# Performance work log

Hardware: AMD Instinct MI355X
Metric: run time of the kernel (lower is better)

Reference implementation:

```python
import jax, jax.numpy as jnp
import numpy as np

B, S, D, V = 2, 2048, 1024, 50257
GAMMA = 1.0
IGNORE = -100


def setup_inputs() -> dict:
    key = jax.random.key(0)
    k1, k2, k3, k4 = jax.random.split(key, 4)
    embeddings = jax.random.normal(k1, (B, S, D), dtype=jnp.float32)
    W = jax.random.normal(k2, (V, D), dtype=jnp.float32) * (D ** -0.5)
    b = jnp.zeros((V,), dtype=jnp.float32)
    labels = jax.random.randint(k3, (B, S), 0, V, dtype=jnp.int64)
    input_ids = jax.random.randint(k4, (B, S), 0, V, dtype=jnp.int64)
    return {"embeddings": embeddings, "W": W, "b": b, "labels": labels, "input_ids": input_ids}


def _focal_loss(embeddings, W, b, labels):
    # logits: [B, S, V]
    logits = jnp.einsum('bsd,vd->bsv', embeddings, W) + b
    shift_logits = logits[:, :-1, :].reshape(-1, V)          # [N, V]
    shift_labels = labels[:, 1:].reshape(-1)                  # [N]
    valid = shift_labels != IGNORE
    safe = jnp.where(valid, shift_labels, 0)
    logp = jax.nn.log_softmax(shift_logits, axis=-1)
    ce = -jnp.take_along_axis(logp, safe[:, None], axis=-1)[:, 0]
    ce = jnp.where(valid, ce, 0.0)                            # ignore_index -> 0 loss
    pt = jax.lax.stop_gradient(jnp.exp(-ce))
    w = (1.0 - pt) ** GAMMA
    alpha = 1.0 / jnp.mean(w)
    loss = alpha * w * ce
    return jnp.mean(loss)


def reference(embeddings, W, b, labels, input_ids):
    return _focal_loss(embeddings, W, b, labels)
```

## Files before the change

### kernel.cpp

```cpp
#include <hip/hip_runtime.h>
#include <hip/hip_bf16.h>
#include <cstdint>

#define SDIM   2048
#define DDIM   1024
#define VDIM   50257
#define VPAD   50432
#define NROWS  4094
#define MPAD   4096
#define NTM    16
#define NTN    197
#define NCHUNK (NTN * 4)
#define NKT    16
#define IGNORE_IDX (-100)
#define NEGBIG (-3.0e38f)
#define SLICE_SH 8192

typedef __bf16 bf16x8 __attribute__((ext_vector_type(8)));
typedef float  f32x4  __attribute__((ext_vector_type(4)));

__device__ static inline unsigned short f2bf(float f) {
    union { float f; uint32_t u; } v; v.f = f;
    uint32_t u = v.u;
    return (unsigned short)((u + 0x7FFFu + ((u >> 16) & 1u)) >> 16);
}

__device__ static inline void gload_lds16(const void* g, void* l) {
    __builtin_amdgcn_global_load_lds(
        (const __attribute__((address_space(1))) unsigned int*)(g),
        (__attribute__((address_space(3))) unsigned int*)(l),
        16, 0, 0);
}

__global__ __launch_bounds__(256) void k_convert_W(const float* __restrict__ W,
                                                   unsigned short* __restrict__ Wb,
                                                   float* __restrict__ acc) {
    if (blockIdx.x == 0 && threadIdx.x < 2) acc[threadIdx.x] = 0.f;
    const int row = blockIdx.x;
    const int c4  = threadIdx.x << 2;
    ushort4 o;
    if (row < VDIM) {
        const float4 f = *(const float4*)(W + (size_t)row * DDIM + c4);
        o.x = f2bf(f.x); o.y = f2bf(f.y); o.z = f2bf(f.z); o.w = f2bf(f.w);
    } else {
        o.x = o.y = o.z = o.w = 0;
    }
    *(ushort4*)(Wb + (size_t)row * DDIM + c4) = o;
}

__global__ __launch_bounds__(256) void k_convert_A(const float* __restrict__ emb,
                                                   unsigned short* __restrict__ Ab) {
    const int row = blockIdx.x;
    const int c4  = threadIdx.x << 2;
    ushort4 o; o.x = o.y = o.z = o.w = 0;
    if (row < NROWS) {
        const int bb = row / 2047;
        const int s  = row - bb * 2047;
        const float4 f = *(const float4*)(emb + ((size_t)bb * SDIM + s) * DDIM + c4);
        o.x = f2bf(f.x); o.y = f2bf(f.y); o.z = f2bf(f.z); o.w = f2bf(f.w);
    }
    *(ushort4*)(Ab + (size_t)row * DDIM + c4) = o;
}

__global__ __launch_bounds__(512, 2) void k_gemm(const unsigned short* __restrict__ Ab,
                                                 const unsigned short* __restrict__ Wb,
                                                 const float* __restrict__ bias,
                                                 float2* __restrict__ Pml) {
    extern __shared__ unsigned short lds[];
    unsigned short* As = lds;
    unsigned short* Bs = lds + 4 * SLICE_SH;

    const int tid  = threadIdx.x;
    const int wave = tid >> 6, lane = tid & 63;
    const int q    = lane & 15, g = lane >> 4;
    const int wr   = wave >> 2;
    const int wc   = wave & 3;

    const int bid0 = (int)blockIdx.x;
    const int bid  = (bid0 & 7) * (NTM * NTN / 8) + (bid0 >> 3);
    const int tm   = bid & 15;
    const int tn   = bid >> 4;
    const size_t arow0 = (size_t)tm * 256;
    const size_t brow0 = (size_t)tn * 256;

    f32x4 acc[8][4];
    const f32x4 zf = {0.f, 0.f, 0.f, 0.f};
#pragma unroll
    for (int i = 0; i < 8; ++i)
#pragma unroll
        for (int j = 0; j < 4; ++j) acc[i][j] = zf;

    auto stage_slice = [&](int kt, int s) {
        const int bufIdx = kt & 1;
        unsigned short* LA = As + (bufIdx * 2 + s) * SLICE_SH;
        unsigned short* LB = Bs + (bufIdx * 2 + s) * SLICE_SH;
#pragma unroll
        for (int j = 0; j < 2; ++j) {
            const int ci  = j * 512 + tid;
            const int row = ((ci >> 3) << 1) + ((ci >> 2) & 1);
            const int cs  = (ci & 3) ^ ((ci >> 3) & 3);
            const size_t goff = (size_t)kt * 64 + s * 32 + cs * 8;
            const size_t ldst = (size_t)(j * 512 + wave * 64) * 8;
            gload_lds16(Ab + (arow0 + row) * DDIM + goff, LA + ldst);
            gload_lds16(Wb + (brow0 + row) * DDIM + goff, LB + ldst);
        }
    };

    auto lds_frag = [&](const unsigned short* SL, int row) -> bf16x8 {
        const int line = row >> 1;
        const int p    = ((row & 1) << 2) + (g ^ (line & 3));
        return *(const bf16x8*)(SL + line * 64 + p * 8);
    };

    auto phase = [&](int bt, int mh, int ks, int stKt, int stS, int vm) {
        const unsigned short* SA = As + (bt * 2 + ks) * SLICE_SH;
        const unsigned short* SB = Bs + (bt * 2 + ks) * SLICE_SH;
        bf16x8 af[4], bfr[4];
#pragma unroll
        for (int fi = 0; fi < 4; ++fi)
            af[fi] = lds_frag(SA, wr * 128 + mh * 64 + fi * 16 + q);
#pragma unroll
        for (int fj = 0; fj < 4; ++fj)
            bfr[fj] = lds_frag(SB, wc * 64 + fj * 16 + q);
        if (stKt >= 0) stage_slice(stKt, stS);
        __builtin_amdgcn_sched_barrier(0);
        __builtin_amdgcn_s_barrier();
        asm volatile("s_waitcnt lgkmcnt(0)" ::: "memory");
        __builtin_amdgcn_sched_barrier(0);
        __builtin_amdgcn_s_setprio(1);
#pragma unroll
        for (int fi = 0; fi < 4; ++fi)
#pragma unroll
            for (int fj = 0; fj < 4; ++fj)
                acc[mh * 4 + fi][fj] = __builtin_amdgcn_mfma_f32_16x16x32_bf16(
                    af[fi], bfr[fj], acc[mh * 4 + fi][fj], 0, 0, 0);
        __builtin_amdgcn_s_setprio(0);
        __builtin_amdgcn_sched_barrier(0);
        if (vm == 8)      { asm volatile("s_waitcnt vmcnt(8)" ::: "memory"); __builtin_amdgcn_sched_barrier(0); }
        else if (vm == 4) { asm volatile("s_waitcnt vmcnt(4)" ::: "memory"); __builtin_amdgcn_sched_barrier(0); }
        else if (vm == 0) { asm volatile("s_waitcnt vmcnt(0)" ::: "memory"); __builtin_amdgcn_sched_barrier(0); }
        __builtin_amdgcn_s_barrier();
    };

    stage_slice(0, 0);
    stage_slice(0, 1);
    stage_slice(1, 0);
    asm volatile("s_waitcnt vmcnt(8)" ::: "memory");
    __builtin_amdgcn_sched_barrier(0);
    __builtin_amdgcn_s_barrier();

#pragma unroll 1
    for (int i = 0; i < 7; ++i) {
        const int t = 2 * i;
        phase(0, 0, 0, t + 1, 1, -1);
        phase(0, 1, 0, -1, 0, 8);
        phase(0, 0, 1, t + 2, 0, -1);
        phase(0, 1, 1, -1, 0, 8);
        phase(1, 0, 0, t + 2, 1, -1);
        phase(1, 1, 0, -1, 0, 8);
        phase(1, 0, 1, t + 3, 0, -1);
        phase(1, 1, 1, -1, 0, 8);
    }
    {
        phase(0, 0, 0, 15, 1, -1);
        phase(0, 1, 0, -1, 0, 8);
        phase(0, 0, 1, -1, 0, -1);
        phase(0, 1, 1, -1, 0, 4);
        phase(1, 0, 0, -1, 0, -1);
        phase(1, 1, 0, -1, 0, 0);
        phase(1, 0, 1, -1, 0, -1);
        phase(1, 1, 1, -1, 0, -1);
    }

    float bv[4]; int colv[4];
#pragma unroll
    for (int fj = 0; fj < 4; ++fj) {
        const int col = tn * 256 + wc * 64 + fj * 16 + q;
        colv[fj] = col;
        bv[fj] = (col < VDIM) ? bias[col] : 0.f;
    }
#pragma unroll
    for (int mf = 0; mf < 8; ++mf) {
#pragma unroll
        for (int r = 0; r < 4; ++r) {
            float vv[4];
#pragma unroll
            for (int fj = 0; fj < 4; ++fj) {
                const float lv = acc[mf][fj][r] + bv[fj];
                vv[fj] = (colv[fj] < VDIM) ? lv : NEGBIG;
            }
            float m = fmaxf(fmaxf(vv[0], vv[1]), fmaxf(vv[2], vv[3]));
#pragma unroll
            for (int mask = 1; mask < 16; mask <<= 1) m = fmaxf(m, __shfl_xor(m, mask));
            float s = __expf(vv[0] - m) + __expf(vv[1] - m) +
                      __expf(vv[2] - m) + __expf(vv[3] - m);
#pragma unroll
            for (int mask = 1; mask < 16; mask <<= 1) s += __shfl_xor(s, mask);
            if (q == ((mf * 4 + r) & 15)) {
                const int rowg = tm * 256 + wr * 128 + mf * 16 + g * 4 + r;
                Pml[(size_t)rowg * NCHUNK + (tn * 4 + wc)] = make_float2(m, s);
            }
        }
    }
}

__global__ __launch_bounds__(256) void k_finalize(const float2* __restrict__ Pml,
                                                  const float* __restrict__ emb,
                                                  const float* __restrict__ W,
                                                  const float* __restrict__ bias,
                                                  const int* __restrict__ labels,
                                                  float* __restrict__ acc) {
    const int r    = blockIdx.x;
    const int tid  = threadIdx.x;
    const int lane = tid & 63, wave = tid >> 6;

    float m = NEGBIG, l = 0.f;
    for (int c = tid; c < NCHUNK; c += 256) {
        const float2 p = Pml[(size_t)r * NCHUNK + c];
        const float mn = fmaxf(m, p.x);
        l = l * __expf(m - mn) + p.y * __expf(p.x - mn);
        m = mn;
    }
#pragma unroll
    for (int mask = 1; mask < 64; mask <<= 1) {
        const float om = __shfl_xor(m, mask);
        const float ol = __shfl_xor(l, mask);
        const float mn = fmaxf(m, om);
        l = l * __expf(m - mn) + ol * __expf(om - mn);
        m = mn;
    }

    const int bb = r / 2047;
    const int s  = r - bb * 2047;
    const int label = labels[bb * SDIM + s + 1];
    const bool valid = (label != IGNORE_IDX);
    const int lab = valid ? label : 0;
    const float* erow = emb + ((size_t)bb * SDIM + s) * DDIM;
    const float* wrow = W + (size_t)lab * DDIM;
    const float4 e  = *(const float4*)(erow + tid * 4);
    const float4 w4 = *(const float4*)(wrow + tid * 4);
    float d = e.x * w4.x + e.y * w4.y + e.z * w4.z + e.w * w4.w;
#pragma unroll
    for (int mask = 1; mask < 64; mask <<= 1) d += __shfl_xor(d, mask);

    __shared__ float sm[4], sl[4], sd[4];
    if (lane == 0) { sm[wave] = m; sl[wave] = l; sd[wave] = d; }
    __syncthreads();
    if (tid == 0) {
        float M = sm[0], L = sl[0];
#pragma unroll
        for (int wv = 1; wv < 4; ++wv) {
            const float mn = fmaxf(M, sm[wv]);
            L = L * __expf(M - mn) + sl[wv] * __expf(sm[wv] - mn);
            M = mn;
        }
        const float dot = sd[0] + sd[1] + sd[2] + sd[3];
        const float lse = M + logf(L);
        const float logit = dot + bias[lab];
        const float ce = valid ? (lse - logit) : 0.f;
        const float pt = __expf(-ce);
        const float w  = valid ? (1.f - pt) : 0.f;
        atomicAdd(acc + 0, w * ce);
        atomicAdd(acc + 1, w);
    }
}

__global__ void k_final(const float* __restrict__ acc, float* __restrict__ out) {
    out[0] = acc[0] / acc[1];
}

extern "C" void kernel_launch(void* const* d_in, const int* in_sizes, int n_in,
                              void* d_out, int out_size, void* d_ws, size_t ws_size,
                              hipStream_t stream) {
    const float* emb    = (const float*)d_in[0];
    const float* W      = (const float*)d_in[1];
    const float* bias   = (const float*)d_in[2];
    const int*   labels = (const int*)d_in[3];

    char* ws = (char*)d_ws;
    const size_t WB = (size_t)VPAD * DDIM * 2;
    const size_t AB = (size_t)MPAD * DDIM * 2;
    const size_t PB = (size_t)MPAD * NCHUNK * 8;
    unsigned short* Wb  = (unsigned short*)ws;
    unsigned short* Ab  = (unsigned short*)(ws + WB);
    float2*         Pml = (float2*)(ws + WB + AB);
    float*          acc = (float*)(ws + WB + AB + PB);

    k_convert_W<<<VPAD, 256, 0, stream>>>(W, Wb, acc);
    k_convert_A<<<MPAD, 256, 0, stream>>>(emb, Ab);
    k_gemm<<<NTM * NTN, 512, 131072, stream>>>(Ab, Wb, bias, Pml);
    k_finalize<<<NROWS, 256, 0, stream>>>(Pml, emb, W, bias, labels, acc);
    k_final<<<1, 1, 0, stream>>>(acc, (float*)d_out);
}
```

Baseline: 954.5 us.

## Restructure GEMM k-loop into 4-deep ring of 32-wide tiles and bucket atomics

The main logits GEMM loop changes from 64-wide k tiles, each split into two slices and processed in eight barrier-separated phases, to 32-wide k tiles held in a 4-entry LDS ring. Each tile is loaded two iterations ahead and both M-halves are computed inside one tile step. This cuts the number of workgroup barriers and explicit waitcnt/sched_barrier fences per k step, aiming to keep MFMA issue denser. It drops the explicit lgkmcnt wait and scheduling barriers, leaving the compiler to order LDS reads. Separately, the per-row focal-loss partial sums are spread over 64 atomic buckets, which the final kernel sums, to reduce same-address atomic contention.

```diff
diff --git a/kernel.cpp b/kernel.cpp
--- a/kernel.cpp
+++ b/kernel.cpp
@@ -11,7 +11,7 @@
 #define NTM    16
 #define NTN    197
 #define NCHUNK (NTN * 4)
-#define NKT    16
+#define NKT    32
 #define IGNORE_IDX (-100)
 #define NEGBIG (-3.0e38f)
 #define SLICE_SH 8192
@@ -35,7 +35,7 @@
 __global__ __launch_bounds__(256) void k_convert_W(const float* __restrict__ W,
                                                    unsigned short* __restrict__ Wb,
                                                    float* __restrict__ acc) {
-    if (blockIdx.x == 0 && threadIdx.x < 2) acc[threadIdx.x] = 0.f;
+    if (blockIdx.x == 0 && threadIdx.x < 128) acc[threadIdx.x] = 0.f;
     const int row = blockIdx.x;
     const int c4  = threadIdx.x << 2;
     ushort4 o;
@@ -90,16 +90,16 @@
 #pragma unroll
         for (int j = 0; j < 4; ++j) acc[i][j] = zf;
 
-    auto stage_slice = [&](int kt, int s) {
-        const int bufIdx = kt & 1;
-        unsigned short* LA = As + (bufIdx * 2 + s) * SLICE_SH;
-        unsigned short* LB = Bs + (bufIdx * 2 + s) * SLICE_SH;
+    auto stage = [&](int kt) {
+        const int b = kt & 3;
+        unsigned short* LA = As + b * SLICE_SH;
+        unsigned short* LB = Bs + b * SLICE_SH;
 #pragma unroll
         for (int j = 0; j < 2; ++j) {
             const int ci  = j * 512 + tid;
             const int row = ((ci >> 3) << 1) + ((ci >> 2) & 1);
             const int cs  = (ci & 3) ^ ((ci >> 3) & 3);
-            const size_t goff = (size_t)kt * 64 + s * 32 + cs * 8;
+            const size_t goff = (size_t)kt * 32 + cs * 8;
             const size_t ldst = (size_t)(j * 512 + wave * 64) * 8;
             gload_lds16(Ab + (arow0 + row) * DDIM + goff, LA + ldst);
             gload_lds16(Wb + (brow0 + row) * DDIM + goff, LB + ldst);
@@ -112,64 +112,55 @@
         return *(const bf16x8*)(SL + line * 64 + p * 8);
     };
 
-    auto phase = [&](int bt, int mh, int ks, int stKt, int stS, int vm) {
-        const unsigned short* SA = As + (bt * 2 + ks) * SLICE_SH;
-        const unsigned short* SB = Bs + (bt * 2 + ks) * SLICE_SH;
+    auto tile = [&](int t, int stKt) {
+        const unsigned short* SA = As + (t & 3) * SLICE_SH;
+        const unsigned short* SB = Bs + (t & 3) * SLICE_SH;
         bf16x8 af[4], bfr[4];
 #pragma unroll
         for (int fi = 0; fi < 4; ++fi)
-            af[fi] = lds_frag(SA, wr * 128 + mh * 64 + fi * 16 + q);
+            af[fi] = lds_frag(SA, wr * 128 + fi * 16 + q);
 #pragma unroll
         for (int fj = 0; fj < 4; ++fj)
             bfr[fj] = lds_frag(SB, wc * 64 + fj * 16 + q);
-        if (stKt >= 0) stage_slice(stKt, stS);
-        __builtin_amdgcn_sched_barrier(0);
+        if (stKt >= 0) stage(stKt);
+        __builtin_amdgcn_s_setprio(1);
+#pragma unroll
+        for (int fi = 0; fi < 4; ++fi)
+#pragma unroll
+            for (int fj = 0; fj < 4; ++fj)
+                acc[fi][fj] = __builtin_amdgcn_mfma_f32_16x16x32_bf16(
+                    af[fi], bfr[fj], acc[fi][fj], 0, 0, 0);
+        __builtin_amdgcn_s_setprio(0);
+#pragma unroll
+        for (int fi = 0; fi < 4; ++fi)
+            af[fi] = lds_frag(SA, wr * 128 + 64 + fi * 16 + q);
+        __builtin_amdgcn_s_setprio(1);
+#pragma unroll
+        for (int fi = 0; fi < 4; ++fi)
+#pragma unroll
+            for (int fj = 0; fj < 4; ++fj)
+                acc[4 + fi][fj] = __builtin_amdgcn_mfma_f32_16x16x32_bf16(
+                    af[fi], bfr[fj], acc[4 + fi][fj], 0, 0, 0);
+        __builtin_amdgcn_s_setprio(0);
+    };
+
+    stage(0);
+    stage(1);
+    asm volatile("s_waitcnt vmcnt(4)" ::: "memory");
+    __builtin_amdgcn_s_barrier();
+
+#pragma unroll 2
+    for (int i = 0; i < NKT / 2; ++i) {
+        const int t = 2 * i;
+        tile(t, (t + 2 < NKT) ? (t + 2) : -1);
+        if (i == NKT / 2 - 1) { asm volatile("s_waitcnt vmcnt(0)" ::: "memory"); }
+        else                  { asm volatile("s_waitcnt vmcnt(4)" ::: "memory"); }
         __builtin_amdgcn_s_barrier();
-        asm volatile("s_waitcnt lgkmcnt(0)" ::: "memory");
-        __builtin_amdgcn_sched_barrier(0);
-        __builtin_amdgcn_s_setprio(1);
-#pragma unroll
-        for (int fi = 0; fi < 4; ++fi)
-#pragma unroll
-            for (int fj = 0; fj < 4; ++fj)
-                acc[mh * 4 + fi][fj] = __builtin_amdgcn_mfma_f32_16x16x32_bf16(
-                    af[fi], bfr[fj], acc[mh * 4 + fi][fj], 0, 0, 0);
-        __builtin_amdgcn_s_setprio(0);
-        __builtin_amdgcn_sched_barrier(0);
-        if (vm == 8)      { asm volatile("s_waitcnt vmcnt(8)" ::: "memory"); __builtin_amdgcn_sched_barrier(0); }
-        else if (vm == 4) { asm volatile("s_waitcnt vmcnt(4)" ::: "memory"); __builtin_amdgcn_sched_barrier(0); }
-        else if (vm == 0) { asm volatile("s_waitcnt vmcnt(0)" ::: "memory"); __builtin_amdgcn_sched_barrier(0); }
-        __builtin_amdgcn_s_barrier();
-    };
-
-    stage_slice(0, 0);
-    stage_slice(0, 1);
-    stage_slice(1, 0);
-    asm volatile("s_waitcnt vmcnt(8)" ::: "memory");
-    __builtin_amdgcn_sched_barrier(0);
-    __builtin_amdgcn_s_barrier();
-
-#pragma unroll 1
-    for (int i = 0; i < 7; ++i) {
-        const int t = 2 * i;
-        phase(0, 0, 0, t + 1, 1, -1);
-        phase(0, 1, 0, -1, 0, 8);
-        phase(0, 0, 1, t + 2, 0, -1);
-        phase(0, 1, 1, -1, 0, 8);
-        phase(1, 0, 0, t + 2, 1, -1);
-        phase(1, 1, 0, -1, 0, 8);
-        phase(1, 0, 1, t + 3, 0, -1);
-        phase(1, 1, 1, -1, 0, 8);
-    }
-    {
-        phase(0, 0, 0, 15, 1, -1);
-        phase(0, 1, 0, -1, 0, 8);
-        phase(0, 0, 1, -1, 0, -1);
-        phase(0, 1, 1, -1, 0, 4);
-        phase(1, 0, 0, -1, 0, -1);
-        phase(1, 1, 0, -1, 0, 0);
-        phase(1, 0, 1, -1, 0, -1);
-        phase(1, 1, 1, -1, 0, -1);
+        tile(t + 1, (t + 3 < NKT) ? (t + 3) : -1);
+        if (i < NKT / 2 - 1) {
+            asm volatile("s_waitcnt vmcnt(4)" ::: "memory");
+            __builtin_amdgcn_s_barrier();
+        }
     }
 
     float bv[4]; int colv[4];
@@ -260,13 +251,17 @@
         const float ce = valid ? (lse - logit) : 0.f;
         const float pt = __expf(-ce);
         const float w  = valid ? (1.f - pt) : 0.f;
-        atomicAdd(acc + 0, w * ce);
-        atomicAdd(acc + 1, w);
+        const int bkt = blockIdx.x & 63;
+        atomicAdd(acc + bkt, w * ce);
+        atomicAdd(acc + 64 + bkt, w);
     }
 }
 
 __global__ void k_final(const float* __restrict__ acc, float* __restrict__ out) {
-    out[0] = acc[0] / acc[1];
+    float num = 0.f, den = 0.f;
+#pragma unroll
+    for (int i = 0; i < 64; ++i) { num += acc[i]; den += acc[64 + i]; }
+    out[0] = num / den;
 }
 
 extern "C" void kernel_launch(void* const* d_in, const int* in_sizes, int n_in,
```

Measured after the change: 834.0 us. 12.6% less time.
